# Kernel optimization log

Hardware: AMD Instinct MI355X
Metric: run time of the kernel (lower is better)

Reference implementation:

```python
import jax, jax.numpy as jnp
import numpy as np

EPS = 1e-5
CONV_THRESHOLD = 0.0


def setup_inputs() -> dict:
    key = jax.random.key(0)
    ks = jax.random.split(key, 16)
    B, F = 65536, 256
    H1, H2 = 1024, 512
    d_in = F + 1  # raw features + 1 scalar conv feature
    inp = {
        "x": jax.random.normal(ks[0], (B, F), dtype=jnp.float32),
        # layer 1: Linear(d_in, H1) + BatchNorm1d(H1)
        "W1": jax.random.normal(ks[1], (d_in, H1), dtype=jnp.float32) * (1.0 / np.sqrt(d_in)),
        "b1": jax.random.normal(ks[2], (H1,), dtype=jnp.float32) * 0.01,
        "g1": jnp.ones((H1,), jnp.float32) + 0.1 * jax.random.normal(ks[3], (H1,), dtype=jnp.float32),
        "be1": jax.random.normal(ks[4], (H1,), dtype=jnp.float32) * 0.01,
        "m1": jax.random.normal(ks[5], (H1,), dtype=jnp.float32) * 0.1,
        "v1": jax.random.uniform(ks[6], (H1,), dtype=jnp.float32, minval=0.5, maxval=1.5),
        # layer 2: Linear(H1, H2) + BatchNorm1d(H2)
        "W2": jax.random.normal(ks[7], (H1, H2), dtype=jnp.float32) * (1.0 / np.sqrt(H1)),
        "b2": jax.random.normal(ks[8], (H2,), dtype=jnp.float32) * 0.01,
        "g2": jnp.ones((H2,), jnp.float32) + 0.1 * jax.random.normal(ks[9], (H2,), dtype=jnp.float32),
        "be2": jax.random.normal(ks[10], (H2,), dtype=jnp.float32) * 0.01,
        "m2": jax.random.normal(ks[11], (H2,), dtype=jnp.float32) * 0.1,
        "v2": jax.random.uniform(ks[12], (H2,), dtype=jnp.float32, minval=0.5, maxval=1.5),
        # output head: Linear(H2, 1)
        "W3": jax.random.normal(ks[13], (H2, 1), dtype=jnp.float32) * (1.0 / np.sqrt(H2)),
        "b3": jax.random.normal(ks[14], (1,), dtype=jnp.float32) * 0.01,
    }
    return inp


def _bn(h, g, be, m, v):
    # eval-mode BatchNorm1d with running statistics
    return g * (h - m) * jax.lax.rsqrt(v + EPS) + be


def reference(x, W1, b1, g1, be1, m1, v1, W2, b2, g2, be2, m2, v2, W3, b3):
    # Batched replacement of the per-sample numpy threshold conv:
    # the Conv filter reduces the whole sample patch with a mean and thresholds it,
    # producing one binary scalar feature per sample.  [B, 1]
    conv_feat = jnp.where(jnp.mean(x, axis=1, keepdims=True) > CONV_THRESHOLD, 1.0, 0.0).astype(x.dtype)
    h = jnp.concatenate([x, conv_feat], axis=1)  # [B, F+1]
    h = jax.nn.relu(_bn(h @ W1 + b1, g1, be1, m1, v1))  # [B, H1]
    h = jax.nn.relu(_bn(h @ W2 + b2, g2, be2, m2, v2))  # [B, H2]
    return jax.nn.sigmoid(h @ W3 + b3)  # [B, 1]
```

## Files before the change

### kernel.cpp

```cpp
#include <hip/hip_runtime.h>
#include <hip/hip_bf16.h>
#include <cstdint>
#include <cstddef>

typedef __bf16 bf16_t;
typedef bf16_t bf16x8 __attribute__((ext_vector_type(8)));
typedef float f32x4 __attribute__((ext_vector_type(4)));

#define BN_EPS 1e-5f

__device__ __forceinline__ void async_load16(const bf16_t* g, bf16_t* lds) {
  __builtin_amdgcn_global_load_lds(
      (__attribute__((address_space(1))) uint32_t*)(g),
      (__attribute__((address_space(3))) uint32_t*)(lds),
      16, 0, 0);
}

__global__ void prep_weights_kernel(const float* __restrict__ W1, const float* __restrict__ W2,
                                    const float* b1, const float* g1, const float* be1,
                                    const float* m1, const float* v1,
                                    const float* b2, const float* g2, const float* be2,
                                    const float* m2, const float* v2,
                                    bf16_t* __restrict__ W1T, bf16_t* __restrict__ W2T,
                                    float* s1, float* t1, float* s2, float* t2,
                                    float* w1last) {
  const int b = blockIdx.x;
  if (b < 192) {
    const float* src;
    bf16_t* dst;
    int R, C, bx, by;
    if (b < 64) { src = W1; dst = W1T; R = 256; C = 1024; bx = b & 15; by = b >> 4; }
    else        { src = W2; dst = W2T; R = 1024; C = 512; bx = (b - 64) & 7; by = (b - 64) >> 3; }
    __shared__ bf16_t tile[64][66];
    const int r0 = by * 64, c0 = bx * 64;
    const int tc = threadIdx.x & 63;
    const int tr4 = threadIdx.x >> 6;
#pragma unroll
    for (int i = 0; i < 16; ++i) {
      int r = i * 4 + tr4;
      tile[r][tc] = (bf16_t)src[(size_t)(r0 + r) * C + c0 + tc];
    }
    __syncthreads();
#pragma unroll
    for (int i = 0; i < 16; ++i) {
      int rr = i * 4 + tr4;
      dst[(size_t)(c0 + rr) * R + r0 + tc] = tile[tc][rr];
    }
  } else {
    for (int i = threadIdx.x; i < 1024; i += 256) {
      float s = g1[i] * rsqrtf(v1[i] + BN_EPS);
      s1[i] = s;
      t1[i] = be1[i] - m1[i] * s + b1[i] * s;
      w1last[i] = W1[256 * 1024 + i];
      if (i < 512) {
        float s2v = g2[i] * rsqrtf(v2[i] + BN_EPS);
        s2[i] = s2v;
        t2[i] = be2[i] - m2[i] * s2v + b2[i] * s2v;
      }
    }
  }
}

__global__ __launch_bounds__(256, 3) void fused_mlp(
    const float* __restrict__ x,
    const bf16_t* __restrict__ W1T, const bf16_t* __restrict__ W2T,
    const float* __restrict__ s1, const float* __restrict__ t1,
    const float* __restrict__ w1last,
    const float* __restrict__ s2, const float* __restrict__ t2,
    const float* __restrict__ W3, const float* __restrict__ b3,
    bf16_t* __restrict__ h1, float* __restrict__ out) {
  __shared__ __align__(16) unsigned char smem[49152];
  const int tid = threadIdx.x;
  const int lane = tid & 63;
  const int w = tid >> 6;
  const int l15 = lane & 15;
  const int quad = lane >> 4;
  const int mTile = blockIdx.x * 64;

  bf16_t* As = (bf16_t*)smem;
  bf16_t* Bs = (bf16_t*)(smem + 32768);
  float* convs = (float*)(smem + 32768);

  {
    const int rsub = lane >> 5;
    const int c = lane & 31;
#pragma unroll
    for (int i = 0; i < 8; ++i) {
      int row = w * 16 + i * 2 + rsub;
      const float* gx = x + (size_t)(mTile + row) * 256 + c * 8;
      const float4 a = *(const float4*)gx;
      const float4 bq = *(const float4*)(gx + 4);
      float s = a.x + a.y + a.z + a.w + bq.x + bq.y + bq.z + bq.w;
      bf16x8 v = {(bf16_t)a.x, (bf16_t)a.y, (bf16_t)a.z, (bf16_t)a.w,
                  (bf16_t)bq.x, (bf16_t)bq.y, (bf16_t)bq.z, (bf16_t)bq.w};
      *(bf16x8*)(As + row * 256 + (c ^ (row & 7)) * 8) = v;
#pragma unroll
      for (int m = 1; m <= 16; m <<= 1) s += __shfl_xor(s, m);
      if (c == 0) convs[row] = (s > 0.0f) ? 1.0f : 0.0f;
    }
  }
  __syncthreads();

  unsigned cmask = 0;
#pragma unroll
  for (int ti = 0; ti < 4; ++ti)
#pragma unroll
    for (int r = 0; r < 4; ++r)
      if (convs[ti * 16 + quad * 4 + r] > 0.5f) cmask |= (1u << (ti * 4 + r));
  __syncthreads();

  bf16_t* BsW = Bs + w * 2048;
  const int srow = lane >> 2;
  const int schunk = (lane & 3) ^ ((lane >> 3) & 3);
  const int rchunk = quad ^ ((l15 >> 1) & 3);

  for (int j = 0; j < 4; ++j) {
    const int colbase = j * 256 + w * 64;
    f32x4 acc[4][4];
#pragma unroll
    for (int i = 0; i < 4; ++i)
#pragma unroll
      for (int t = 0; t < 4; ++t) {
        f32x4 z = {0.f, 0.f, 0.f, 0.f};
        acc[i][t] = z;
      }

    const bf16_t* gB = W1T + (size_t)(colbase + srow) * 256 + schunk * 8;

#pragma unroll
    for (int i = 0; i < 4; ++i)
      async_load16(gB + (size_t)(i * 16) * 256, BsW + i * 512 + lane * 8);

    for (int ks = 0; ks < 8; ++ks) {
      asm volatile("s_waitcnt vmcnt(0)" ::: "memory");

      bf16x8 af[4], bfr[4];
#pragma unroll
      for (int tj = 0; tj < 4; ++tj)
        bfr[tj] = *(const bf16x8*)(BsW + (tj * 16 + l15) * 32 + rchunk * 8);
#pragma unroll
      for (int ti = 0; ti < 4; ++ti)
        af[ti] = *(const bf16x8*)(As + (ti * 16 + l15) * 256 + ((ks * 4 + quad) ^ (l15 & 7)) * 8);

      asm volatile("s_waitcnt lgkmcnt(0)" ::: "memory");
      if (ks < 7) {
#pragma unroll
        for (int i = 0; i < 4; ++i)
          async_load16(gB + (size_t)(i * 16) * 256 + (ks + 1) * 32, BsW + i * 512 + lane * 8);
      }

      __builtin_amdgcn_s_setprio(1);
#pragma unroll
      for (int ti = 0; ti < 4; ++ti)
#pragma unroll
        for (int tj = 0; tj < 4; ++tj)
          acc[ti][tj] = __builtin_amdgcn_mfma_f32_16x16x32_bf16(af[ti], bfr[tj], acc[ti][tj], 0, 0, 0);
      __builtin_amdgcn_s_setprio(0);
    }

    float sc[4], tcv[4], wl[4];
#pragma unroll
    for (int tj = 0; tj < 4; ++tj) {
      int c = colbase + tj * 16 + l15;
      sc[tj] = s1[c];
      tcv[tj] = t1[c];
      wl[tj] = w1last[c];
    }
#pragma unroll
    for (int ti = 0; ti < 4; ++ti)
#pragma unroll
      for (int r = 0; r < 4; ++r) {
        int row = mTile + ti * 16 + quad * 4 + r;
        size_t base = (size_t)row * 1024 + colbase;
        const float cfv = ((cmask >> (ti * 4 + r)) & 1u) ? 1.0f : 0.0f;
#pragma unroll
        for (int tj = 0; tj < 4; ++tj) {
          float z = acc[ti][tj][r] + cfv * wl[tj];
          z = fmaxf(z * sc[tj] + tcv[tj], 0.f);
          h1[base + tj * 16 + l15] = (bf16_t)z;
        }
      }
  }

  asm volatile("s_waitcnt vmcnt(0)" ::: "memory");

  bf16_t* A2 = (bf16_t*)smem;
  bf16_t* B2 = (bf16_t*)(smem + 8192);
  float* outW = (float*)(smem + 40960);
  const int rchunk8 = rchunk * 8;
  const int sColSwz = schunk * 8;

  float rowpv[4][4];
#pragma unroll
  for (int ti = 0; ti < 4; ++ti)
#pragma unroll
    for (int r = 0; r < 4; ++r) rowpv[ti][r] = 0.f;

  for (int nt = 0; nt < 2; ++nt) {
    __syncthreads();

    const bf16_t* gA = h1 + (size_t)(mTile + w * 16 + srow) * 1024 + sColSwz;
    const bf16_t* gB2 = W2T + (size_t)(nt * 256 + w * 64 + srow) * 1024 + sColSwz;

    f32x4 acc2[4][4];
#pragma unroll
    for (int i = 0; i < 4; ++i)
#pragma unroll
      for (int t = 0; t < 4; ++t) {
        f32x4 z = {0.f, 0.f, 0.f, 0.f};
        acc2[i][t] = z;
      }

#define STAGE2(buf, k0)                                                       \
  do {                                                                        \
    async_load16(gA + (k0), A2 + (buf)*2048 + w * 512 + lane * 8);            \
    async_load16(gB2 + (k0), B2 + (buf)*8192 + w * 2048 + lane * 8);          \
    async_load16(gB2 + (size_t)16 * 1024 + (k0),                              \
                 B2 + (buf)*8192 + w * 2048 + 512 + lane * 8);                \
    async_load16(gB2 + (size_t)32 * 1024 + (k0),                              \
                 B2 + (buf)*8192 + w * 2048 + 1024 + lane * 8);               \
    async_load16(gB2 + (size_t)48 * 1024 + (k0),                              \
                 B2 + (buf)*8192 + w * 2048 + 1536 + lane * 8);               \
  } while (0)

    STAGE2(0, 0);
    int buf = 0;
    for (int t = 0; t < 32; ++t) {
      if (t < 31) {
        STAGE2(buf ^ 1, (t + 1) * 32);
        asm volatile("s_waitcnt vmcnt(5)" ::: "memory");
      } else {
        asm volatile("s_waitcnt vmcnt(0)" ::: "memory");
      }
      asm volatile("s_barrier" ::: "memory");

      bf16x8 af[4], bfr[4];
#pragma unroll
      for (int ti = 0; ti < 4; ++ti)
        af[ti] = *(const bf16x8*)(A2 + buf * 2048 + (ti * 16 + l15) * 32 + rchunk8);
#pragma unroll
      for (int tj = 0; tj < 4; ++tj)
        bfr[tj] = *(const bf16x8*)(B2 + buf * 8192 + (w * 64 + tj * 16 + l15) * 32 + rchunk8);

      __builtin_amdgcn_s_setprio(1);
#pragma unroll
      for (int ti = 0; ti < 4; ++ti)
#pragma unroll
        for (int tj = 0; tj < 4; ++tj)
          acc2[ti][tj] = __builtin_amdgcn_mfma_f32_16x16x32_bf16(af[ti], bfr[tj], acc2[ti][tj], 0, 0, 0);
      __builtin_amdgcn_s_setprio(0);

      asm volatile("s_barrier" ::: "memory");
      buf ^= 1;
    }
#undef STAGE2

    float sc[4], tcs[4], w3c[4];
#pragma unroll
    for (int tj = 0; tj < 4; ++tj) {
      int c = nt * 256 + w * 64 + tj * 16 + l15;
      sc[tj] = s2[c];
      tcs[tj] = t2[c];
      w3c[tj] = W3[c];
    }
#pragma unroll
    for (int ti = 0; ti < 4; ++ti)
#pragma unroll
      for (int r = 0; r < 4; ++r) {
        float pv = 0.f;
#pragma unroll
        for (int tj = 0; tj < 4; ++tj) {
          float z = fmaxf(acc2[ti][tj][r] * sc[tj] + tcs[tj], 0.f);
          pv += z * w3c[tj];
        }
#pragma unroll
        for (int m = 1; m <= 8; m <<= 1) pv += __shfl_xor(pv, m);
        rowpv[ti][r] += pv;
      }
  }

  if (l15 == 0) {
#pragma unroll
    for (int ti = 0; ti < 4; ++ti)
#pragma unroll
      for (int r = 0; r < 4; ++r)
        outW[w * 64 + ti * 16 + quad * 4 + r] = rowpv[ti][r];
  }
  __syncthreads();
  if (tid < 64) {
    float z = outW[tid] + outW[64 + tid] + outW[128 + tid] + outW[192 + tid] + b3[0];
    out[mTile + tid] = 1.0f / (1.0f + expf(-z));
  }
}

extern "C" void kernel_launch(void* const* d_in, const int* in_sizes, int n_in,
                              void* d_out, int out_size, void* d_ws, size_t ws_size,
                              hipStream_t stream) {
  const float* x = (const float*)d_in[0];
  const float* W1 = (const float*)d_in[1];
  const float* b1 = (const float*)d_in[2];
  const float* g1 = (const float*)d_in[3];
  const float* be1 = (const float*)d_in[4];
  const float* m1 = (const float*)d_in[5];
  const float* v1 = (const float*)d_in[6];
  const float* W2 = (const float*)d_in[7];
  const float* b2 = (const float*)d_in[8];
  const float* g2 = (const float*)d_in[9];
  const float* be2 = (const float*)d_in[10];
  const float* m2 = (const float*)d_in[11];
  const float* v2 = (const float*)d_in[12];
  const float* W3 = (const float*)d_in[13];
  const float* b3 = (const float*)d_in[14];
  float* out = (float*)d_out;

  char* p = (char*)d_ws;
  bf16_t* h1 = (bf16_t*)p;       p += (size_t)65536 * 1024 * 2;
  float* partials = (float*)p;   p += (size_t)4 * 65536 * 4;
  bf16_t* W1T = (bf16_t*)p;      p += (size_t)1024 * 256 * 2;
  bf16_t* W2T = (bf16_t*)p;      p += (size_t)512 * 1024 * 2;
  float* w1last = (float*)p;     p += 1024 * 4;
  float* s1 = (float*)p;         p += 1024 * 4;
  float* t1 = (float*)p;         p += 1024 * 4;
  float* s2 = (float*)p;         p += 512 * 4;
  float* t2 = (float*)p;         p += 512 * 4;
  (void)partials;

  prep_weights_kernel<<<193, 256, 0, stream>>>(W1, W2, b1, g1, be1, m1, v1,
                                               b2, g2, be2, m2, v2,
                                               W1T, W2T, s1, t1, s2, t2, w1last);

  fused_mlp<<<1024, 256, 0, stream>>>(x, W1T, W2T, s1, t1, w1last,
                                      s2, t2, W3, b3, h1, out);
}
```

Measured before the change: 261.5 us.

## Keep layer-1 activations in LDS and stream layer-2 GEMM per K-chunk

Layer 1 is now computed in 256-column chunks written into a swizzled LDS buffer, and each chunk is consumed right away by a layer-2 partial GEMM whose accumulators (64x512 per block) stay in registers. This removes the global h1 round trip (write plus re-read of 128 MB in bf16). Layer-2 weights are now read directly from global memory into registers instead of being staged through LDS. LDS grows to 72 KB and register pressure rises, so launch bounds drop to 2 blocks per CU, which lowers occupancy.

```diff
diff --git a/kernel.cpp b/kernel.cpp
--- a/kernel.cpp
+++ b/kernel.cpp
@@ -61,15 +61,15 @@
   }
 }
 
-__global__ __launch_bounds__(256, 3) void fused_mlp(
+__global__ __launch_bounds__(256, 2) void fused_mlp(
     const float* __restrict__ x,
     const bf16_t* __restrict__ W1T, const bf16_t* __restrict__ W2T,
     const float* __restrict__ s1, const float* __restrict__ t1,
     const float* __restrict__ w1last,
     const float* __restrict__ s2, const float* __restrict__ t2,
     const float* __restrict__ W3, const float* __restrict__ b3,
-    bf16_t* __restrict__ h1, float* __restrict__ out) {
-  __shared__ __align__(16) unsigned char smem[49152];
+    float* __restrict__ out) {
+  __shared__ __align__(16) unsigned char smem[73728];
   const int tid = threadIdx.x;
   const int lane = tid & 63;
   const int w = tid >> 6;
@@ -78,25 +78,27 @@
   const int mTile = blockIdx.x * 64;
 
   bf16_t* As = (bf16_t*)smem;
-  bf16_t* Bs = (bf16_t*)(smem + 32768);
+  bf16_t* h1c = (bf16_t*)(smem + 32768);
   float* convs = (float*)(smem + 32768);
+  bf16_t* B1s = (bf16_t*)(smem + 65536);
+  float* outW = (float*)(smem + 65536);
 
   {
     const int rsub = lane >> 5;
-    const int c = lane & 31;
+    const int cc = lane & 31;
 #pragma unroll
     for (int i = 0; i < 8; ++i) {
       int row = w * 16 + i * 2 + rsub;
-      const float* gx = x + (size_t)(mTile + row) * 256 + c * 8;
+      const float* gx = x + (size_t)(mTile + row) * 256 + cc * 8;
       const float4 a = *(const float4*)gx;
       const float4 bq = *(const float4*)(gx + 4);
       float s = a.x + a.y + a.z + a.w + bq.x + bq.y + bq.z + bq.w;
       bf16x8 v = {(bf16_t)a.x, (bf16_t)a.y, (bf16_t)a.z, (bf16_t)a.w,
                   (bf16_t)bq.x, (bf16_t)bq.y, (bf16_t)bq.z, (bf16_t)bq.w};
-      *(bf16x8*)(As + row * 256 + (c ^ (row & 7)) * 8) = v;
+      *(bf16x8*)(As + row * 256 + (cc ^ (row & 7)) * 8) = v;
 #pragma unroll
       for (int m = 1; m <= 16; m <<= 1) s += __shfl_xor(s, m);
-      if (c == 0) convs[row] = (s > 0.0f) ? 1.0f : 0.0f;
+      if (cc == 0) convs[row] = (s > 0.0f) ? 1.0f : 0.0f;
     }
   }
   __syncthreads();
@@ -107,178 +109,140 @@
 #pragma unroll
     for (int r = 0; r < 4; ++r)
       if (convs[ti * 16 + quad * 4 + r] > 0.5f) cmask |= (1u << (ti * 4 + r));
-  __syncthreads();
-
-  bf16_t* BsW = Bs + w * 2048;
+
+  bf16_t* B1w = B1s + w * 1024;
   const int srow = lane >> 2;
   const int schunk = (lane & 3) ^ ((lane >> 3) & 3);
   const int rchunk = quad ^ ((l15 >> 1) & 3);
 
-  for (int j = 0; j < 4; ++j) {
-    const int colbase = j * 256 + w * 64;
-    f32x4 acc[4][4];
-#pragma unroll
-    for (int i = 0; i < 4; ++i)
-#pragma unroll
-      for (int t = 0; t < 4; ++t) {
-        f32x4 z = {0.f, 0.f, 0.f, 0.f};
-        acc[i][t] = z;
-      }
-
-    const bf16_t* gB = W1T + (size_t)(colbase + srow) * 256 + schunk * 8;
-
-#pragma unroll
-    for (int i = 0; i < 4; ++i)
-      async_load16(gB + (size_t)(i * 16) * 256, BsW + i * 512 + lane * 8);
-
-    for (int ks = 0; ks < 8; ++ks) {
-      asm volatile("s_waitcnt vmcnt(0)" ::: "memory");
-
-      bf16x8 af[4], bfr[4];
-#pragma unroll
-      for (int tj = 0; tj < 4; ++tj)
-        bfr[tj] = *(const bf16x8*)(BsW + (tj * 16 + l15) * 32 + rchunk * 8);
+  f32x4 acc2[4][8];
+#pragma unroll
+  for (int i = 0; i < 4; ++i)
+#pragma unroll
+    for (int j = 0; j < 8; ++j) {
+      f32x4 z = {0.f, 0.f, 0.f, 0.f};
+      acc2[i][j] = z;
+    }
+
+  for (int c = 0; c < 4; ++c) {
+#pragma unroll
+    for (int h = 0; h < 2; ++h) {
+      const int colbase = c * 256 + w * 64 + h * 32;
+      f32x4 acc1[4][2];
+#pragma unroll
+      for (int i = 0; i < 4; ++i)
+#pragma unroll
+        for (int t = 0; t < 2; ++t) {
+          f32x4 z = {0.f, 0.f, 0.f, 0.f};
+          acc1[i][t] = z;
+        }
+
+      const bf16_t* gB1 = W1T + (size_t)(colbase + srow) * 256 + schunk * 8;
+
+#pragma unroll
+      for (int i = 0; i < 2; ++i)
+        async_load16(gB1 + (size_t)(i * 16) * 256, B1w + i * 512 + lane * 8);
+
+      for (int ks = 0; ks < 8; ++ks) {
+        asm volatile("s_waitcnt vmcnt(0)" ::: "memory");
+
+        bf16x8 af[4], bfr[2];
+#pragma unroll
+        for (int tj = 0; tj < 2; ++tj)
+          bfr[tj] = *(const bf16x8*)(B1w + (tj * 16 + l15) * 32 + rchunk * 8);
+#pragma unroll
+        for (int ti = 0; ti < 4; ++ti)
+          af[ti] = *(const bf16x8*)(As + (ti * 16 + l15) * 256 +
+                                    ((ks * 4 + quad) ^ (l15 & 7)) * 8);
+
+        asm volatile("s_waitcnt lgkmcnt(0)" ::: "memory");
+        if (ks < 7) {
+#pragma unroll
+          for (int i = 0; i < 2; ++i)
+            async_load16(gB1 + (size_t)(i * 16) * 256 + (ks + 1) * 32,
+                         B1w + i * 512 + lane * 8);
+        }
+
+#pragma unroll
+        for (int ti = 0; ti < 4; ++ti)
+#pragma unroll
+          for (int tj = 0; tj < 2; ++tj)
+            acc1[ti][tj] = __builtin_amdgcn_mfma_f32_16x16x32_bf16(af[ti], bfr[tj], acc1[ti][tj], 0, 0, 0);
+      }
+
+      if (h == 0) __syncthreads();
+
+      float sc1[2], tc1[2], wl1[2];
+#pragma unroll
+      for (int tj = 0; tj < 2; ++tj) {
+        int ccol = colbase + tj * 16 + l15;
+        sc1[tj] = s1[ccol];
+        tc1[tj] = t1[ccol];
+        wl1[tj] = w1last[ccol];
+      }
 #pragma unroll
       for (int ti = 0; ti < 4; ++ti)
-        af[ti] = *(const bf16x8*)(As + (ti * 16 + l15) * 256 + ((ks * 4 + quad) ^ (l15 & 7)) * 8);
-
-      asm volatile("s_waitcnt lgkmcnt(0)" ::: "memory");
-      if (ks < 7) {
-#pragma unroll
-        for (int i = 0; i < 4; ++i)
-          async_load16(gB + (size_t)(i * 16) * 256 + (ks + 1) * 32, BsW + i * 512 + lane * 8);
-      }
-
+#pragma unroll
+        for (int r = 0; r < 4; ++r) {
+          const int rowl = ti * 16 + quad * 4 + r;
+          const float cfv = ((cmask >> (ti * 4 + r)) & 1u) ? 1.0f : 0.0f;
+#pragma unroll
+          for (int tj = 0; tj < 2; ++tj) {
+            float z = acc1[ti][tj][r] + cfv * wl1[tj];
+            z = fmaxf(z * sc1[tj] + tc1[tj], 0.f);
+            const int colc = w * 64 + h * 32 + tj * 16 + l15;
+            const int c8 = (colc >> 3) ^ (rowl & 7);
+            h1c[rowl * 256 + c8 * 8 + (l15 & 7)] = (bf16_t)z;
+          }
+        }
+    }
+    __syncthreads();
+
+    const bf16_t* gB2 = W2T + (size_t)(w * 128 + l15) * 1024 + c * 256 + quad * 8;
+#pragma unroll
+    for (int s = 0; s < 8; ++s) {
+      bf16x8 af2[4], bfr2[8];
+#pragma unroll
+      for (int tj = 0; tj < 8; ++tj)
+        bfr2[tj] = *(const bf16x8*)(gB2 + (size_t)(tj * 16) * 1024 + s * 32);
+#pragma unroll
+      for (int ti = 0; ti < 4; ++ti)
+        af2[ti] = *(const bf16x8*)(h1c + (ti * 16 + l15) * 256 +
+                                   ((s * 4 + quad) ^ (l15 & 7)) * 8);
       __builtin_amdgcn_s_setprio(1);
 #pragma unroll
       for (int ti = 0; ti < 4; ++ti)
 #pragma unroll
-        for (int tj = 0; tj < 4; ++tj)
-          acc[ti][tj] = __builtin_amdgcn_mfma_f32_16x16x32_bf16(af[ti], bfr[tj], acc[ti][tj], 0, 0, 0);
+        for (int tj = 0; tj < 8; ++tj)
+          acc2[ti][tj] = __builtin_amdgcn_mfma_f32_16x16x32_bf16(af2[ti], bfr2[tj], acc2[ti][tj], 0, 0, 0);
       __builtin_amdgcn_s_setprio(0);
     }
-
-    float sc[4], tcv[4], wl[4];
-#pragma unroll
-    for (int tj = 0; tj < 4; ++tj) {
-      int c = colbase + tj * 16 + l15;
-      sc[tj] = s1[c];
-      tcv[tj] = t1[c];
-      wl[tj] = w1last[c];
-    }
-#pragma unroll
-    for (int ti = 0; ti < 4; ++ti)
-#pragma unroll
-      for (int r = 0; r < 4; ++r) {
-        int row = mTile + ti * 16 + quad * 4 + r;
-        size_t base = (size_t)row * 1024 + colbase;
-        const float cfv = ((cmask >> (ti * 4 + r)) & 1u) ? 1.0f : 0.0f;
-#pragma unroll
-        for (int tj = 0; tj < 4; ++tj) {
-          float z = acc[ti][tj][r] + cfv * wl[tj];
-          z = fmaxf(z * sc[tj] + tcv[tj], 0.f);
-          h1[base + tj * 16 + l15] = (bf16_t)z;
-        }
-      }
-  }
-
-  asm volatile("s_waitcnt vmcnt(0)" ::: "memory");
-
-  bf16_t* A2 = (bf16_t*)smem;
-  bf16_t* B2 = (bf16_t*)(smem + 8192);
-  float* outW = (float*)(smem + 40960);
-  const int rchunk8 = rchunk * 8;
-  const int sColSwz = schunk * 8;
-
+  }
+
+  float sc[8], tcs[8], w3c[8];
+#pragma unroll
+  for (int tj = 0; tj < 8; ++tj) {
+    int ccol = w * 128 + tj * 16 + l15;
+    sc[tj] = s2[ccol];
+    tcs[tj] = t2[ccol];
+    w3c[tj] = W3[ccol];
+  }
+  __syncthreads();
   float rowpv[4][4];
 #pragma unroll
   for (int ti = 0; ti < 4; ++ti)
 #pragma unroll
-    for (int r = 0; r < 4; ++r) rowpv[ti][r] = 0.f;
-
-  for (int nt = 0; nt < 2; ++nt) {
-    __syncthreads();
-
-    const bf16_t* gA = h1 + (size_t)(mTile + w * 16 + srow) * 1024 + sColSwz;
-    const bf16_t* gB2 = W2T + (size_t)(nt * 256 + w * 64 + srow) * 1024 + sColSwz;
-
-    f32x4 acc2[4][4];
-#pragma unroll
-    for (int i = 0; i < 4; ++i)
-#pragma unroll
-      for (int t = 0; t < 4; ++t) {
-        f32x4 z = {0.f, 0.f, 0.f, 0.f};
-        acc2[i][t] = z;
-      }
-
-#define STAGE2(buf, k0)                                                       \
-  do {                                                                        \
-    async_load16(gA + (k0), A2 + (buf)*2048 + w * 512 + lane * 8);            \
-    async_load16(gB2 + (k0), B2 + (buf)*8192 + w * 2048 + lane * 8);          \
-    async_load16(gB2 + (size_t)16 * 1024 + (k0),                              \
-                 B2 + (buf)*8192 + w * 2048 + 512 + lane * 8);                \
-    async_load16(gB2 + (size_t)32 * 1024 + (k0),                              \
-                 B2 + (buf)*8192 + w * 2048 + 1024 + lane * 8);               \
-    async_load16(gB2 + (size_t)48 * 1024 + (k0),                              \
-                 B2 + (buf)*8192 + w * 2048 + 1536 + lane * 8);               \
-  } while (0)
-
-    STAGE2(0, 0);
-    int buf = 0;
-    for (int t = 0; t < 32; ++t) {
-      if (t < 31) {
-        STAGE2(buf ^ 1, (t + 1) * 32);
-        asm volatile("s_waitcnt vmcnt(5)" ::: "memory");
-      } else {
-        asm volatile("s_waitcnt vmcnt(0)" ::: "memory");
-      }
-      asm volatile("s_barrier" ::: "memory");
-
-      bf16x8 af[4], bfr[4];
-#pragma unroll
-      for (int ti = 0; ti < 4; ++ti)
-        af[ti] = *(const bf16x8*)(A2 + buf * 2048 + (ti * 16 + l15) * 32 + rchunk8);
-#pragma unroll
-      for (int tj = 0; tj < 4; ++tj)
-        bfr[tj] = *(const bf16x8*)(B2 + buf * 8192 + (w * 64 + tj * 16 + l15) * 32 + rchunk8);
-
-      __builtin_amdgcn_s_setprio(1);
-#pragma unroll
-      for (int ti = 0; ti < 4; ++ti)
-#pragma unroll
-        for (int tj = 0; tj < 4; ++tj)
-          acc2[ti][tj] = __builtin_amdgcn_mfma_f32_16x16x32_bf16(af[ti], bfr[tj], acc2[ti][tj], 0, 0, 0);
-      __builtin_amdgcn_s_setprio(0);
-
-      asm volatile("s_barrier" ::: "memory");
-      buf ^= 1;
-    }
-#undef STAGE2
-
-    float sc[4], tcs[4], w3c[4];
-#pragma unroll
-    for (int tj = 0; tj < 4; ++tj) {
-      int c = nt * 256 + w * 64 + tj * 16 + l15;
-      sc[tj] = s2[c];
-      tcs[tj] = t2[c];
-      w3c[tj] = W3[c];
-    }
-#pragma unroll
-    for (int ti = 0; ti < 4; ++ti)
-#pragma unroll
-      for (int r = 0; r < 4; ++r) {
-        float pv = 0.f;
-#pragma unroll
-        for (int tj = 0; tj < 4; ++tj) {
-          float z = fmaxf(acc2[ti][tj][r] * sc[tj] + tcs[tj], 0.f);
-          pv += z * w3c[tj];
-        }
-#pragma unroll
-        for (int m = 1; m <= 8; m <<= 1) pv += __shfl_xor(pv, m);
-        rowpv[ti][r] += pv;
-      }
-  }
-
+    for (int r = 0; r < 4; ++r) {
+      float pv = 0.f;
+#pragma unroll
+      for (int tj = 0; tj < 8; ++tj) {
+        float z = fmaxf(acc2[ti][tj][r] * sc[tj] + tcs[tj], 0.f);
+        pv += z * w3c[tj];
+      }
+#pragma unroll
+      for (int m = 1; m <= 8; m <<= 1) pv += __shfl_xor(pv, m);
+      rowpv[ti][r] = pv;
+    }
   if (l15 == 0) {
 #pragma unroll
     for (int ti = 0; ti < 4; ++ti)
@@ -323,6 +287,7 @@
   float* t1 = (float*)p;         p += 1024 * 4;
   float* s2 = (float*)p;         p += 512 * 4;
   float* t2 = (float*)p;         p += 512 * 4;
+  (void)h1;
   (void)partials;
 
   prep_weights_kernel<<<193, 256, 0, stream>>>(W1, W2, b1, g1, be1, m1, v1,
@@ -330,5 +295,5 @@
                                                W1T, W2T, s1, t1, s2, t2, w1last);
 
   fused_mlp<<<1024, 256, 0, stream>>>(x, W1T, W2T, s1, t1, w1last,
-                                      s2, t2, W3, b3, h1, out);
-}
+                                      s2, t2, W3, b3, out);
+}
```

Result: slower. 308.6 us (+18.0%).
